# Optimization experiments

Hardware: AMD Instinct MI355X
Metric: run time of the kernel (lower is better)

The kernel has to match this reference:

```python
import jax, jax.numpy as jnp
import numpy as np

N_NODES = 50000
N_EDGES = 1000000
N_GRAPHS = 256
ORIG = 92
ATOM = 64
NBR = 41
EPS = 1e-5


def _bn_train(h, gamma, beta):
    # BatchNorm1d in training mode: batch stats, biased variance
    mu = h.mean(axis=0)
    var = jnp.var(h, axis=0)
    return (h - mu) * jax.lax.rsqrt(var + EPS) * gamma + beta


def setup_inputs() -> dict:
    key = jax.random.key(0)
    ks = jax.random.split(key, 16)
    inp = {
        "x": jax.random.normal(ks[0], (N_NODES, ORIG), dtype=jnp.float32),
        "edge_attr": jax.random.normal(ks[1], (N_EDGES, NBR), dtype=jnp.float32),
        "lower_f": jax.random.normal(ks[2], (N_NODES, ATOM), dtype=jnp.float32),
        "edge_index": jax.random.randint(ks[3], (2, N_EDGES), 0, N_NODES, dtype=jnp.int32),
        "batch": jnp.sort(jax.random.randint(ks[4], (N_NODES,), 0, N_GRAPHS, dtype=jnp.int32)),
        # params
        "emb_W": jax.random.normal(ks[5], (ORIG, ATOM), dtype=jnp.float32) / np.sqrt(ORIG),
        "emb_b": jnp.zeros((ATOM,), dtype=jnp.float32),
        "fc_W": jax.random.normal(ks[6], (2 * ATOM + NBR, 2 * ATOM), dtype=jnp.float32) / np.sqrt(2 * ATOM + NBR),
        "fc_b": jnp.zeros((2 * ATOM,), dtype=jnp.float32),
        "bn1_g": jnp.ones((2 * ATOM,), dtype=jnp.float32),
        "bn1_b": jnp.zeros((2 * ATOM,), dtype=jnp.float32),
        "bn2_g": jnp.ones((ATOM,), dtype=jnp.float32),
        "bn2_b": jnp.zeros((ATOM,), dtype=jnp.float32),
        "att_W": jax.random.normal(ks[7], (ATOM, 1), dtype=jnp.float32) / np.sqrt(ATOM),
        "att_b": jnp.zeros((1,), dtype=jnp.float32),
        "out_W": jax.random.normal(ks[8], (ATOM, 1), dtype=jnp.float32) / np.sqrt(ATOM),
        "out_b": jnp.zeros((1,), dtype=jnp.float32),
    }
    return inp


def reference(x, edge_attr, lower_f, emb_W, emb_b, fc_W, fc_b, bn1_g, bn1_b,
              bn2_g, bn2_b, att_W, att_b, out_W, out_b, edge_index, batch):
    # embedding + lower-level features
    atom_fea = x @ emb_W + emb_b + lower_f  # [N, ATOM]

    # CGConv: gather endpoints, concat with edge features
    src, dst = edge_index[0], edge_index[1]
    total = jnp.concatenate([atom_fea[src], atom_fea[dst], edge_attr], axis=-1)  # [E, 2A+NBR]
    gated = _bn_train(total @ fc_W + fc_b, bn1_g, bn1_b)  # [E, 2A]
    nbr_filter, nbr_core = gated[:, :ATOM], gated[:, ATOM:]
    msg = jax.nn.sigmoid(nbr_filter) * jax.nn.softplus(nbr_core)  # [E, A]
    summed = jax.ops.segment_sum(msg, src, num_segments=N_NODES)  # [N, A]
    atom_out = _bn_train(summed, bn2_g, bn2_b)

    # SiLU + attentional aggregation per graph
    h = jax.nn.silu(atom_out)  # [N, A]
    logits = (h @ att_W + att_b)[:, 0]  # [N]
    seg_max = jax.ops.segment_max(logits, batch, num_segments=N_GRAPHS)
    e = jnp.exp(logits - seg_max[batch])
    denom = jax.ops.segment_sum(e, batch, num_segments=N_GRAPHS)
    alpha = e / denom[batch]  # [N]
    crys = jax.ops.segment_sum(alpha[:, None] * h, batch, num_segments=N_GRAPHS)  # [G, A]
    crys_fea = crys @ out_W + out_b  # [G, 1]
    return atom_out, crys_fea
```

## Files before the change

### kernel.cpp

```cpp
#include <hip/hip_runtime.h>
#include <math.h>

#define NN 50000
#define NE 1000000
#define NG 256
#define ORIGD 92
#define NBRD 41
#define NSPREAD 32
#define SCAN_B 256

typedef unsigned short u16;
typedef __attribute__((ext_vector_type(8))) short short8;
typedef __attribute__((ext_vector_type(4))) float f32x4;

#define OFF_AFB     0
#define OFF_SUMMED  1600000
#define OFF_WT      4800000
#define OFF_BN1SPR  4812288
#define OFF_BN1SC   4820480
#define OFF_BN2ACC  4820736
#define OFF_BN2SC   4820864
#define OFF_ELOG    4820992
#define OFF_SEGMAX  4870992
#define OFF_DENOM   4871248
#define OFF_CNT     4871504
#define OFF_PTR     4921504
#define OFF_HEAD    4971504
#define OFF_BSUM    5021504
#define OFF_BOFS    5021760
#define OFF_EIDX    5022016
#define OFF_H       6022016
#define OFF_T2_END  70022016
#define OFF_P       70022016
#define OFF_T3_END  82822016

__device__ __forceinline__ u16 f2b(float f) {
    unsigned u = __float_as_uint(f);
    return (u16)((u + 0x7FFFu + ((u >> 16) & 1u)) >> 16);
}
__device__ __forceinline__ float b2f(u16 u) {
    return __uint_as_float(((unsigned)u) << 16);
}
__device__ __forceinline__ float gate(float f, float cc) {
    float sig = __builtin_amdgcn_rcpf(1.f + __expf(-f));
    float sp  = fmaxf(cc, 0.f) + __logf(1.f + __expf(-fabsf(cc)));
    return sig * sp;
}
__device__ __forceinline__ float fsilu(float x) {
    return x * __builtin_amdgcn_rcpf(1.f + __expf(-x));
}

__global__ __launch_bounds__(256) void k_embed(
    const float* __restrict__ x, const float* __restrict__ lf,
    const float* __restrict__ W, const float* __restrict__ b,
    u16* __restrict__ afb)
{
    int gid = blockIdx.x * 256 + threadIdx.x;
    int n = gid >> 6, c = gid & 63;
    const float* xr = x + (long)n * ORIGD;
    float acc = b[c] + lf[gid];
#pragma unroll 4
    for (int k = 0; k < ORIGD; k++)
        acc = fmaf(xr[k], W[k * 64 + c], acc);
    afb[gid] = f2b(acc);
}

__global__ void k_prepw(const float* __restrict__ fcW, u16* __restrict__ wT)
{
    int i = blockIdx.x * 256 + threadIdx.x;
    int j = i / 192, k = i - j * 192;
    wT[i] = (k < 169) ? f2b(fcW[k * 128 + j]) : (u16)0;
}

__global__ void k_prepw2(const float* __restrict__ fcW, u16* __restrict__ wT3,
                         u16* __restrict__ wP)
{
    int i = blockIdx.x * 256 + threadIdx.x;
    if (i < 8192) {
        int j = i >> 6, k = i & 63;
        wT3[i] = (k < NBRD) ? f2b(fcW[(128 + k) * 128 + j]) : (u16)0;
    } else {
        int i2 = i - 8192;
        int j = i2 >> 6, k = i2 & 63;
        int row = (j < 128) ? k : (64 + k);
        wP[i2] = f2b(fcW[row * 128 + (j & 127)]);
    }
}

__global__ __launch_bounds__(256) void k_pnode(
    const u16* __restrict__ afb, const u16* __restrict__ wP, float* __restrict__ P)
{
    __shared__ __align__(16) u16 sB[64 * 72];
    const int tid = threadIdx.x;
    const int n0 = blockIdx.x * 64;

    for (int i = tid; i < 512; i += 256) {
        int r = i >> 3, c = i & 7;
        int n = n0 + r;
        short8 v = {0,0,0,0,0,0,0,0};
        if (n < NN) v = *(const short8*)(afb + (long)n * 64 + c * 8);
        *(short8*)(sB + r * 72 + c * 8) = v;
    }
    __syncthreads();

    const int lane = tid & 63, w = tid >> 6;
    const int n16 = lane & 15, quad = lane >> 4;
    short8 A[4][2];
#pragma unroll
    for (int m = 0; m < 4; m++) {
        const u16* base = wP + (16 * (w + 4 * m) + n16) * 64 + quad * 8;
        A[m][0] = *(const short8*)(base);
        A[m][1] = *(const short8*)(base + 32);
    }
    for (int t = 0; t < 4; t++) {
        const u16* row = sB + (16 * t + n16) * 72 + quad * 8;
        short8 b0 = *(const short8*)(row);
        short8 b1 = *(const short8*)(row + 32);
        int n = n0 + 16 * t + n16;
#pragma unroll
        for (int m = 0; m < 4; m++) {
            f32x4 acc = {0.f, 0.f, 0.f, 0.f};
            acc = __builtin_amdgcn_mfma_f32_16x16x32_bf16(A[m][0], b0, acc, 0, 0, 0);
            acc = __builtin_amdgcn_mfma_f32_16x16x32_bf16(A[m][1], b1, acc, 0, 0, 0);
            if (n < NN) {
                int j = 16 * (w + 4 * m) + 4 * quad;
                *(f32x4*)(P + (long)n * 256 + j) = acc;
            }
        }
    }
}

__global__ void k_hist(const int* __restrict__ ei, int* __restrict__ cnt)
{
    int e = blockIdx.x * 256 + threadIdx.x;
    if (e < NE) atomicAdd(&cnt[ei[e]], 1);
}

__global__ void k_partial(const int* __restrict__ cnt, int* __restrict__ lofs,
                          int* __restrict__ bsum)
{
    __shared__ int sd[SCAN_B];
    int t = threadIdx.x, b = blockIdx.x, n = b * SCAN_B + t;
    int v = (n < NN) ? cnt[n] : 0;
    sd[t] = v; __syncthreads();
    for (int o = 1; o < SCAN_B; o <<= 1) {
        int x = (t >= o) ? sd[t - o] : 0;
        __syncthreads();
        sd[t] += x;
        __syncthreads();
    }
    if (n < NN) lofs[n] = sd[t] - v;
    if (t == SCAN_B - 1) bsum[b] = sd[t];
}

__global__ void k_scanb(const int* __restrict__ bsum, int* __restrict__ bofs, int nb)
{
    __shared__ int sd[256];
    int t = threadIdx.x;
    int v = (t < nb) ? bsum[t] : 0;
    sd[t] = v; __syncthreads();
    for (int o = 1; o < 256; o <<= 1) {
        int x = (t >= o) ? sd[t - o] : 0;
        __syncthreads();
        sd[t] += x;
        __syncthreads();
    }
    bofs[t] = sd[t] - v;
}

__global__ void k_addofs(int* __restrict__ ptr, const int* __restrict__ bofs,
                         int* __restrict__ head)
{
    int n = blockIdx.x * 256 + threadIdx.x;
    if (n < NN) {
        int p = ptr[n] + bofs[n >> 8];
        ptr[n] = p; head[n] = p;
    }
}

__global__ void k_fill(const int* __restrict__ ei, int* __restrict__ head,
                       int* __restrict__ eidx)
{
    int e = blockIdx.x * 256 + threadIdx.x;
    if (e < NE) {
        int pos = atomicAdd(&head[ei[e]], 1);
        eidx[pos] = e;
    }
}

__global__ __launch_bounds__(256) void k_gemm_h2(
    const float* __restrict__ ea, const int* __restrict__ ei,
    const u16* __restrict__ wT3, const float* __restrict__ P,
    u16* __restrict__ h, float* __restrict__ spread)
{
    __shared__ __align__(16) u16 sTl[64 * 72];
    __shared__ int sSrc[64], sDst[64];
    const int tid = threadIdx.x;
    const int e0 = blockIdx.x * 64;

    if (tid < 64) sSrc[tid] = ei[e0 + tid];
    else if (tid < 128) sDst[tid - 64] = ei[NE + e0 + tid - 64];

    for (int i = tid; i < 64 * 64; i += 256) {
        int e = i >> 6, c = i & 63;
        float v = (c < NBRD) ? ea[(long)(e0 + e) * NBRD + c] : 0.f;
        sTl[e * 72 + c] = f2b(v);
    }
    __syncthreads();

    const int lane = tid & 63, w = tid >> 6;
    const int n16 = lane & 15, quad = lane >> 4;

    short8 A0[2], A1[2];
    {
        const u16* b0 = wT3 + (16 * w + n16) * 64 + quad * 8;
        const u16* b1 = wT3 + (16 * (w + 4) + n16) * 64 + quad * 8;
        A0[0] = *(const short8*)(b0);  A0[1] = *(const short8*)(b0 + 32);
        A1[0] = *(const short8*)(b1);  A1[1] = *(const short8*)(b1 + 32);
    }

    const int j0 = 16 * w + 4 * quad;
    float s0[4] = {0,0,0,0}, q0[4] = {0,0,0,0}, s1[4] = {0,0,0,0}, q1[4] = {0,0,0,0};

    for (int t = 0; t < 4; t++) {
        const int ge16 = 16 * t + n16;
        const int src = sSrc[ge16], dst = sDst[ge16];
        const float* pS = P + (long)src * 256;
        const float* pD = P + (long)dst * 256 + 128;
        f32x4 g0 = *(const f32x4*)(pS + j0);
        f32x4 g1 = *(const f32x4*)(pS + 64 + j0);
        f32x4 g2 = *(const f32x4*)(pD + j0);
        f32x4 g3 = *(const f32x4*)(pD + 64 + j0);

        const u16* row = sTl + ge16 * 72 + quad * 8;
        short8 b0 = *(const short8*)(row);
        short8 b1 = *(const short8*)(row + 32);
        f32x4 acc0 = {0.f, 0.f, 0.f, 0.f}, acc1 = {0.f, 0.f, 0.f, 0.f};
        acc0 = __builtin_amdgcn_mfma_f32_16x16x32_bf16(A0[0], b0, acc0, 0, 0, 0);
        acc0 = __builtin_amdgcn_mfma_f32_16x16x32_bf16(A0[1], b1, acc0, 0, 0, 0);
        acc1 = __builtin_amdgcn_mfma_f32_16x16x32_bf16(A1[0], b0, acc1, 0, 0, 0);
        acc1 = __builtin_amdgcn_mfma_f32_16x16x32_bf16(A1[1], b1, acc1, 0, 0, 0);

        u16 hv0[4], hv1[4];
#pragma unroll
        for (int r = 0; r < 4; r++) {
            float u0 = acc0[r] + g0[r] + g2[r];
            float u1 = acc1[r] + g1[r] + g3[r];
            s0[r] += u0; q0[r] = fmaf(u0, u0, q0[r]);
            s1[r] += u1; q1[r] = fmaf(u1, u1, q1[r]);
            hv0[r] = f2b(u0); hv1[r] = f2b(u1);
        }
        int ge = e0 + ge16;
        u16* hp = h + (long)ge * 128 + j0;
        ushort4 v0 = make_ushort4(hv0[0], hv0[1], hv0[2], hv0[3]);
        ushort4 v1 = make_ushort4(hv1[0], hv1[1], hv1[2], hv1[3]);
        *(ushort4*)hp = v0;
        *(ushort4*)(hp + 64) = v1;
    }

#pragma unroll
    for (int m = 1; m < 16; m <<= 1) {
#pragma unroll
        for (int r = 0; r < 4; r++) {
            s0[r] += __shfl_xor(s0[r], m); q0[r] += __shfl_xor(q0[r], m);
            s1[r] += __shfl_xor(s1[r], m); q1[r] += __shfl_xor(q1[r], m);
        }
    }
    if (n16 == 0) {
        float* sp = spread + (blockIdx.x & (NSPREAD - 1)) * 256;
#pragma unroll
        for (int r = 0; r < 4; r++) {
            atomicAdd(sp + j0 + r,       s0[r]);
            atomicAdd(sp + 128 + j0 + r, q0[r]);
            atomicAdd(sp + 64 + j0 + r,  s1[r]);
            atomicAdd(sp + 192 + j0 + r, q1[r]);
        }
    }
}

__global__ __launch_bounds__(256) void k_gemm_h(
    const u16* __restrict__ afb, const float* __restrict__ ea,
    const int* __restrict__ ei, const u16* __restrict__ wT,
    u16* __restrict__ h, float* __restrict__ spread)
{
    __shared__ __align__(16) u16 sTl[64 * 200];
    __shared__ int sSrc[64], sDst[64];
    const int tid = threadIdx.x;
    const int e0 = blockIdx.x * 64;

    if (tid < 64) sSrc[tid] = ei[e0 + tid];
    else if (tid < 128) sDst[tid - 64] = ei[NE + e0 + tid - 64];
    __syncthreads();

    for (int i = tid; i < 1024; i += 256) {
        int e = i >> 4, q = i & 15;
        const u16* g = (q < 8) ? (afb + (long)sSrc[e] * 64 + q * 8)
                               : (afb + (long)sDst[e] * 64 + (q - 8) * 8);
        *(short8*)(sTl + e * 200 + q * 8) = *(const short8*)g;
    }
    for (int i = tid; i < 64 * 64; i += 256) {
        int e = i >> 6, c = i & 63;
        float v = (c < NBRD) ? ea[(long)(e0 + e) * NBRD + c] : 0.f;
        sTl[e * 200 + 128 + c] = f2b(v);
    }
    __syncthreads();

    const int lane = tid & 63, w = tid >> 6;
    const int n16 = lane & 15, quad = lane >> 4;

    short8 A0[6], A1[6];
    {
        const u16* b0 = wT + (16 * w + n16) * 192 + quad * 8;
        const u16* b1 = wT + (16 * (w + 4) + n16) * 192 + quad * 8;
#pragma unroll
        for (int ks = 0; ks < 6; ks++) {
            A0[ks] = *(const short8*)(b0 + ks * 32);
            A1[ks] = *(const short8*)(b1 + ks * 32);
        }
    }

    const int j0 = 16 * w + 4 * quad;
    float s0[4] = {0,0,0,0}, q0[4] = {0,0,0,0}, s1[4] = {0,0,0,0}, q1[4] = {0,0,0,0};

    for (int t = 0; t < 4; t++) {
        const u16* row = sTl + (16 * t + n16) * 200 + quad * 8;
        f32x4 acc0 = {0.f, 0.f, 0.f, 0.f}, acc1 = {0.f, 0.f, 0.f, 0.f};
#pragma unroll
        for (int ks = 0; ks < 6; ks++) {
            short8 b = *(const short8*)(row + ks * 32);
            acc0 = __builtin_amdgcn_mfma_f32_16x16x32_bf16(A0[ks], b, acc0, 0, 0, 0);
            acc1 = __builtin_amdgcn_mfma_f32_16x16x32_bf16(A1[ks], b, acc1, 0, 0, 0);
        }
#pragma unroll
        for (int r = 0; r < 4; r++) {
            s0[r] += acc0[r]; q0[r] = fmaf(acc0[r], acc0[r], q0[r]);
            s1[r] += acc1[r]; q1[r] = fmaf(acc1[r], acc1[r], q1[r]);
        }
        int ge = e0 + 16 * t + n16;
        u16* hp = h + (long)ge * 128 + j0;
        ushort4 v0 = make_ushort4(f2b(acc0[0]), f2b(acc0[1]), f2b(acc0[2]), f2b(acc0[3]));
        ushort4 v1 = make_ushort4(f2b(acc1[0]), f2b(acc1[1]), f2b(acc1[2]), f2b(acc1[3]));
        *(ushort4*)hp = v0;
        *(ushort4*)(hp + 64) = v1;
    }

#pragma unroll
    for (int m = 1; m < 16; m <<= 1) {
#pragma unroll
        for (int r = 0; r < 4; r++) {
            s0[r] += __shfl_xor(s0[r], m); q0[r] += __shfl_xor(q0[r], m);
            s1[r] += __shfl_xor(s1[r], m); q1[r] += __shfl_xor(q1[r], m);
        }
    }
    if (n16 == 0) {
        float* sp = spread + (blockIdx.x & (NSPREAD - 1)) * 256;
#pragma unroll
        for (int r = 0; r < 4; r++) {
            atomicAdd(sp + j0 + r,       s0[r]);
            atomicAdd(sp + 128 + j0 + r, q0[r]);
            atomicAdd(sp + 64 + j0 + r,  s1[r]);
            atomicAdd(sp + 192 + j0 + r, q1[r]);
        }
    }
}

template <int MODE>
__global__ __launch_bounds__(256) void k_gemm(
    const u16* __restrict__ afb, const float* __restrict__ ea,
    const int* __restrict__ ei, const u16* __restrict__ wT,
    const float* __restrict__ sc, float* __restrict__ outbuf)
{
    __shared__ __align__(16) u16 sTl[64 * 200];
    __shared__ int sSrc[64], sDst[64];
    const int tid = threadIdx.x;
    const int e0 = blockIdx.x * 64;

    if (tid < 64) sSrc[tid] = ei[e0 + tid];
    else if (tid < 128) sDst[tid - 64] = ei[NE + e0 + tid - 64];
    __syncthreads();
    for (int i = tid; i < 1024; i += 256) {
        int e = i >> 4, q = i & 15;
        const u16* g = (q < 8) ? (afb + (long)sSrc[e] * 64 + q * 8)
                               : (afb + (long)sDst[e] * 64 + (q - 8) * 8);
        *(short8*)(sTl + e * 200 + q * 8) = *(const short8*)g;
    }
    for (int i = tid; i < 64 * 64; i += 256) {
        int e = i >> 6, c = i & 63;
        float v = (c < NBRD) ? ea[(long)(e0 + e) * NBRD + c] : 0.f;
        sTl[e * 200 + 128 + c] = f2b(v);
    }
    __syncthreads();

    const int lane = tid & 63, w = tid >> 6;
    const int n16 = lane & 15, quad = lane >> 4;
    short8 A0[6], A1[6];
    {
        const u16* b0 = wT + (16 * w + n16) * 192 + quad * 8;
        const u16* b1 = wT + (16 * (w + 4) + n16) * 192 + quad * 8;
#pragma unroll
        for (int ks = 0; ks < 6; ks++) {
            A0[ks] = *(const short8*)(b0 + ks * 32);
            A1[ks] = *(const short8*)(b1 + ks * 32);
        }
    }
    const int j0 = 16 * w + 4 * quad;
    float s0[4] = {0,0,0,0}, q0[4] = {0,0,0,0}, s1[4] = {0,0,0,0}, q1[4] = {0,0,0,0};
    float scf[4], shf[4], scc[4], shc[4];
    if (MODE == 1) {
#pragma unroll
        for (int r = 0; r < 4; r++) {
            scf[r] = sc[j0 + r];        shf[r] = sc[128 + j0 + r];
            scc[r] = sc[64 + j0 + r];   shc[r] = sc[192 + j0 + r];
        }
    }
    for (int t = 0; t < 4; t++) {
        const u16* row = sTl + (16 * t + n16) * 200 + quad * 8;
        f32x4 acc0 = {0.f, 0.f, 0.f, 0.f}, acc1 = {0.f, 0.f, 0.f, 0.f};
#pragma unroll
        for (int ks = 0; ks < 6; ks++) {
            short8 b = *(const short8*)(row + ks * 32);
            acc0 = __builtin_amdgcn_mfma_f32_16x16x32_bf16(A0[ks], b, acc0, 0, 0, 0);
            acc1 = __builtin_amdgcn_mfma_f32_16x16x32_bf16(A1[ks], b, acc1, 0, 0, 0);
        }
        if (MODE == 0) {
#pragma unroll
            for (int r = 0; r < 4; r++) {
                s0[r] += acc0[r]; q0[r] = fmaf(acc0[r], acc0[r], q0[r]);
                s1[r] += acc1[r]; q1[r] = fmaf(acc1[r], acc1[r], q1[r]);
            }
        } else {
            int src = sSrc[16 * t + n16];
            float* dst = outbuf + (long)src * 64 + j0;
#pragma unroll
            for (int r = 0; r < 4; r++) {
                float f  = fmaf(acc0[r], scf[r], shf[r]);
                float cc = fmaf(acc1[r], scc[r], shc[r]);
                atomicAdd(dst + r, gate(f, cc));
            }
        }
    }
    if (MODE == 0) {
#pragma unroll
        for (int m = 1; m < 16; m <<= 1) {
#pragma unroll
            for (int r = 0; r < 4; r++) {
                s0[r] += __shfl_xor(s0[r], m); q0[r] += __shfl_xor(q0[r], m);
                s1[r] += __shfl_xor(s1[r], m); q1[r] += __shfl_xor(q1[r], m);
            }
        }
        if (n16 == 0) {
            float* sp = outbuf + (blockIdx.x & (NSPREAD - 1)) * 256;
#pragma unroll
            for (int r = 0; r < 4; r++) {
                atomicAdd(sp + j0 + r,       s0[r]);
                atomicAdd(sp + 128 + j0 + r, q0[r]);
                atomicAdd(sp + 64 + j0 + r,  s1[r]);
                atomicAdd(sp + 192 + j0 + r, q1[r]);
            }
        }
    }
}

__global__ void k_bn1fin(const float* __restrict__ spread,
                         const float* __restrict__ g, const float* __restrict__ b,
                         float* __restrict__ sc)
{
    int c = threadIdx.x;
    float s = 0.f, q = 0.f;
    for (int k = 0; k < NSPREAD; k++) { s += spread[k * 256 + c]; q += spread[k * 256 + 128 + c]; }
    float mean_acc = s / (float)NE;
    float var = q / (float)NE - mean_acc * mean_acc;
    float scale = g[c] * rsqrtf(var + 1e-5f);
    sc[c] = scale;
    sc[128 + c] = b[c] - mean_acc * scale;
}

__global__ __launch_bounds__(256) void k_scatter(
    const u16* __restrict__ h, const int* __restrict__ ptr,
    const int* __restrict__ cnt, const int* __restrict__ eidx,
    const float* __restrict__ sc, float* __restrict__ summed)
{
    int tid = threadIdx.x;
    int n = blockIdx.x * 4 + (tid >> 6);
    int l = tid & 63;
    int es = l & 7, cg = l >> 3;

    float4 a0 = *(const float4*)(sc + cg * 8);
    float4 a1 = *(const float4*)(sc + cg * 8 + 4);
    float4 b0 = *(const float4*)(sc + 128 + cg * 8);
    float4 b1 = *(const float4*)(sc + 128 + cg * 8 + 4);
    float4 c0 = *(const float4*)(sc + 64 + cg * 8);
    float4 c1 = *(const float4*)(sc + 64 + cg * 8 + 4);
    float4 d0 = *(const float4*)(sc + 192 + cg * 8);
    float4 d1 = *(const float4*)(sc + 192 + cg * 8 + 4);
    float scf[8] = {a0.x,a0.y,a0.z,a0.w,a1.x,a1.y,a1.z,a1.w};
    float shf[8] = {b0.x,b0.y,b0.z,b0.w,b1.x,b1.y,b1.z,b1.w};
    float scc[8] = {c0.x,c0.y,c0.z,c0.w,c1.x,c1.y,c1.z,c1.w};
    float shc[8] = {d0.x,d0.y,d0.z,d0.w,d1.x,d1.y,d1.z,d1.w};

    int p0 = ptr[n], deg = cnt[n];
    float acc[8] = {0,0,0,0,0,0,0,0};
    for (int i = 0; i < deg; i += 8) {
        int idx = i + es;
        bool valid = idx < deg;
        int e = eidx[p0 + (valid ? idx : 0)];
        const u16* hr = h + (long)e * 128;
        short8 f8 = *(const short8*)(hr + cg * 8);
        short8 c8 = *(const short8*)(hr + 64 + cg * 8);
#pragma unroll
        for (int j = 0; j < 8; j++) {
            float f  = fmaf(b2f((u16)f8[j]), scf[j], shf[j]);
            float cc = fmaf(b2f((u16)c8[j]), scc[j], shc[j]);
            float g  = gate(f, cc);
            acc[j] += valid ? g : 0.f;
        }
    }
#pragma unroll
    for (int m = 1; m < 8; m <<= 1)
#pragma unroll
        for (int j = 0; j < 8; j++) acc[j] += __shfl_xor(acc[j], m);
    if (es == 0) {
        float* sp = summed + (long)n * 64 + cg * 8;
        float4 v0 = {acc[0], acc[1], acc[2], acc[3]};
        float4 v1 = {acc[4], acc[5], acc[6], acc[7]};
        *(float4*)sp = v0;
        *(float4*)(sp + 4) = v1;
    }
}

__global__ __launch_bounds__(256) void k_bn2stats(const float* __restrict__ summed,
                                                  float* __restrict__ acc2)
{
    int tid = threadIdx.x; int c = tid & 63; int sub = tid >> 6;
    float s = 0.f, q = 0.f;
    for (int r = blockIdx.x * 4 + sub; r < NN; r += 4 * 128) {
        float v = summed[(long)r * 64 + c]; s += v; q = fmaf(v, v, q);
    }
    __shared__ float rs[256], rq[256];
    rs[tid] = s; rq[tid] = q; __syncthreads();
    if (tid < 64) {
        s = rs[tid] + rs[tid + 64] + rs[tid + 128] + rs[tid + 192];
        q = rq[tid] + rq[tid + 64] + rq[tid + 128] + rq[tid + 192];
        atomicAdd(&acc2[tid], s);
        atomicAdd(&acc2[64 + tid], q);
    }
}

__global__ void k_bn2fin(const float* __restrict__ acc2,
                         const float* __restrict__ g, const float* __restrict__ b,
                         float* __restrict__ sc2, const float* __restrict__ outb,
                         float* __restrict__ out)
{
    int c = threadIdx.x;
    if (c < 64) {
        float mean = acc2[c] / (float)NN;
        float var = acc2[64 + c] / (float)NN - mean * mean;
        float scale = g[c] * rsqrtf(var + 1e-5f);
        sc2[c] = scale;
        sc2[64 + c] = b[c] - mean * scale;
    }
    out[(long)NN * 64 + c] = outb[0];
}

__global__ __launch_bounds__(256) void k_nodepost(
    const float* __restrict__ summed, const float* __restrict__ sc2,
    const float* __restrict__ attW, const float* __restrict__ attb,
    const int* __restrict__ batch, float* __restrict__ out,
    float* __restrict__ elog, unsigned* __restrict__ segmax)
{
    int tid = threadIdx.x; int n = blockIdx.x * 4 + (tid >> 6); int c = tid & 63;
    float v = summed[(long)n * 64 + c];
    float ao = fmaf(v, sc2[c], sc2[64 + c]);
    out[(long)n * 64 + c] = ao;
    float h = fsilu(ao);
    float p = h * attW[c];
#pragma unroll
    for (int off = 32; off; off >>= 1) p += __shfl_down(p, off, 64);
    if (c == 0) {
        float logit = p + attb[0];
        elog[n] = logit;
        unsigned u = __float_as_uint(logit);
        u = (u & 0x80000000u) ? ~u : (u | 0x80000000u);
        atomicMax(&segmax[batch[n]], u);
    }
}

__global__ void k_denom(const int* __restrict__ batch,
                        const unsigned* __restrict__ segmax,
                        float* __restrict__ elog, float* __restrict__ denom)
{
    int n = blockIdx.x * 256 + threadIdx.x;
    if (n >= NN) return;
    int b = batch[n];
    unsigned u = segmax[b];
    u = (u & 0x80000000u) ? (u & 0x7FFFFFFFu) : ~u;
    float e = __expf(elog[n] - __uint_as_float(u));
    elog[n] = e;
    atomicAdd(&denom[b], e);
}

__global__ __launch_bounds__(256) void k_crys(
    const float* __restrict__ atom_out, const float* __restrict__ elog,
    const float* __restrict__ denom, const int* __restrict__ batch,
    const float* __restrict__ outW, float* __restrict__ out)
{
    int tid = threadIdx.x; int n = blockIdx.x * 4 + (tid >> 6); int l = tid & 63;
    int b = batch[n];
    float alpha = elog[n] / denom[b];
    float ao = atom_out[(long)n * 64 + l];
    float p = fsilu(ao) * outW[l];
#pragma unroll
    for (int off = 32; off; off >>= 1) p += __shfl_down(p, off, 64);
    if (l == 0) atomicAdd(&out[(long)NN * 64 + b], alpha * p);
}

extern "C" void kernel_launch(void* const* d_in, const int* in_sizes, int n_in,
                              void* d_out, int out_size, void* d_ws, size_t ws_size,
                              hipStream_t stream)
{
    const float* x    = (const float*)d_in[0];
    const float* eatt = (const float*)d_in[1];
    const float* lf   = (const float*)d_in[2];
    const int*   ei   = (const int*)d_in[3];
    const int*   batch= (const int*)d_in[4];
    const float* embW = (const float*)d_in[5];
    const float* embB = (const float*)d_in[6];
    const float* fcW  = (const float*)d_in[7];
    const float* bn1g = (const float*)d_in[9];
    const float* bn1b = (const float*)d_in[10];
    const float* bn2g = (const float*)d_in[11];
    const float* bn2b = (const float*)d_in[12];
    const float* attW = (const float*)d_in[13];
    const float* attB = (const float*)d_in[14];
    const float* outW = (const float*)d_in[15];
    const float* outB = (const float*)d_in[16];
    float* out = (float*)d_out;
    float* ws  = (float*)d_ws;

    u16* afb  = (u16*)(ws + OFF_AFB);
    u16* wT   = (u16*)(ws + OFF_WT);
    int* cnt  = (int*)(ws + OFF_CNT);
    int* ptr  = (int*)(ws + OFF_PTR);
    int* head = (int*)(ws + OFF_HEAD);
    int* bsum = (int*)(ws + OFF_BSUM);
    int* bofs = (int*)(ws + OFF_BOFS);
    int* eidx = (int*)(ws + OFF_EIDX);
    u16* h    = (u16*)(ws + OFF_H);

    const bool t3 = ws_size >= (size_t)OFF_T3_END * sizeof(float);
    const bool t2 = ws_size >= (size_t)OFF_T2_END * sizeof(float);

    k_embed<<<12500, 256, 0, stream>>>(x, lf, embW, embB, afb);

    if (t3) {
        u16* wT3 = wT;
        u16* wP  = wT + 8192;
        float* P = ws + OFF_P;
        k_prepw2<<<96, 256, 0, stream>>>(fcW, wT3, wP);
        hipMemsetAsync(ws + OFF_BN1SPR, 0,
                       (size_t)(OFF_PTR - OFF_BN1SPR) * sizeof(float), stream);
        k_hist<<<(NE + 255) / 256, 256, 0, stream>>>(ei, cnt);
        k_partial<<<(NN + SCAN_B - 1) / SCAN_B, SCAN_B, 0, stream>>>(cnt, ptr, bsum);
        k_scanb<<<1, 256, 0, stream>>>(bsum, bofs, (NN + SCAN_B - 1) / SCAN_B);
        k_addofs<<<(NN + 255) / 256, 256, 0, stream>>>(ptr, bofs, head);
        k_fill<<<(NE + 255) / 256, 256, 0, stream>>>(ei, head, eidx);
        k_pnode<<<(NN + 63) / 64, 256, 0, stream>>>(afb, wP, P);
        k_gemm_h2<<<NE / 64, 256, 0, stream>>>(eatt, ei, wT3, P, h, ws + OFF_BN1SPR);
        k_bn1fin<<<1, 128, 0, stream>>>(ws + OFF_BN1SPR, bn1g, bn1b, ws + OFF_BN1SC);
        k_scatter<<<NN / 4, 256, 0, stream>>>(h, ptr, cnt, eidx, ws + OFF_BN1SC,
                                              ws + OFF_SUMMED);
    } else if (t2) {
        k_prepw<<<96, 256, 0, stream>>>(fcW, wT);
        hipMemsetAsync(ws + OFF_BN1SPR, 0,
                       (size_t)(OFF_PTR - OFF_BN1SPR) * sizeof(float), stream);
        k_hist<<<(NE + 255) / 256, 256, 0, stream>>>(ei, cnt);
        k_partial<<<(NN + SCAN_B - 1) / SCAN_B, SCAN_B, 0, stream>>>(cnt, ptr, bsum);
        k_scanb<<<1, 256, 0, stream>>>(bsum, bofs, (NN + SCAN_B - 1) / SCAN_B);
        k_addofs<<<(NN + 255) / 256, 256, 0, stream>>>(ptr, bofs, head);
        k_fill<<<(NE + 255) / 256, 256, 0, stream>>>(ei, head, eidx);
        k_gemm_h<<<NE / 64, 256, 0, stream>>>(afb, eatt, ei, wT, h, ws + OFF_BN1SPR);
        k_bn1fin<<<1, 128, 0, stream>>>(ws + OFF_BN1SPR, bn1g, bn1b, ws + OFF_BN1SC);
        k_scatter<<<NN / 4, 256, 0, stream>>>(h, ptr, cnt, eidx, ws + OFF_BN1SC,
                                              ws + OFF_SUMMED);
    } else {
        k_prepw<<<96, 256, 0, stream>>>(fcW, wT);
        hipMemsetAsync(ws + OFF_SUMMED, 0,
                       (size_t)(OFF_PTR - OFF_SUMMED) * sizeof(float), stream);
        k_gemm<0><<<NE / 64, 256, 0, stream>>>(afb, eatt, ei, wT, ws + OFF_BN1SC,
                                               ws + OFF_BN1SPR);
        k_bn1fin<<<1, 128, 0, stream>>>(ws + OFF_BN1SPR, bn1g, bn1b, ws + OFF_BN1SC);
        k_gemm<1><<<NE / 64, 256, 0, stream>>>(afb, eatt, ei, wT, ws + OFF_BN1SC,
                                               ws + OFF_SUMMED);
    }

    k_bn2stats<<<128, 256, 0, stream>>>(ws + OFF_SUMMED, ws + OFF_BN2ACC);
    k_bn2fin<<<1, 256, 0, stream>>>(ws + OFF_BN2ACC, bn2g, bn2b, ws + OFF_BN2SC,
                                    outB, out);
    k_nodepost<<<12500, 256, 0, stream>>>(ws + OFF_SUMMED, ws + OFF_BN2SC, attW, attB,
                                          batch, out, ws + OFF_ELOG,
                                          (unsigned*)(ws + OFF_SEGMAX));
    k_denom<<<196, 256, 0, stream>>>(batch, (const unsigned*)(ws + OFF_SEGMAX),
                                     ws + OFF_ELOG, ws + OFF_DENOM);
    k_crys<<<12500, 256, 0, stream>>>(out, ws + OFF_ELOG, ws + OFF_DENOM, batch,
                                      outW, out);
}
```

Baseline: 1.241 ms.

## Compute edge GEMM in src-sorted order and pre-convert edge_attr to bf16

Adds a new path that writes h in CSR (src-sorted) order, so the scatter reads contiguous rows directly instead of indirecting through eidx. Edge attributes are first converted to a padded 48-wide bf16 buffer, so the GEMM loads aligned short8 vectors per edge. The fill kernel now also records src and dst per sorted position. The gathers in the GEMM become irregular over eaB and the dst rows of P, and the path needs roughly 100 MB more workspace; if that workspace is not available, the old path runs.

```diff
diff --git a/kernel.cpp b/kernel.cpp
--- a/kernel.cpp
+++ b/kernel.cpp
@@ -33,6 +33,10 @@
 #define OFF_T2_END  70022016
 #define OFF_P       70022016
 #define OFF_T3_END  82822016
+#define OFF_SRCC    82822016
+#define OFF_DSTC    83822016
+#define OFF_EAB     84822016
+#define OFF_T4_END  108822016
 
 __device__ __forceinline__ u16 f2b(float f) {
     unsigned u = __float_as_uint(f);
@@ -87,6 +91,23 @@
     }
 }
 
+__global__ __launch_bounds__(256) void k_prepea(const float* __restrict__ ea,
+                                                u16* __restrict__ eaB)
+{
+    int gid = blockIdx.x * 256 + threadIdx.x;
+    if (gid >= NE * 6) return;
+    int e = gid / 6, q = gid - e * 6;
+    const float* row = ea + (long)e * NBRD;
+    int c0 = q * 8;
+    short8 v;
+#pragma unroll
+    for (int j = 0; j < 8; j++) {
+        int c = c0 + j;
+        v[j] = (c < NBRD) ? (short)f2b(row[c]) : (short)0;
+    }
+    *(short8*)(eaB + (long)e * 48 + c0) = v;
+}
+
 __global__ __launch_bounds__(256) void k_pnode(
     const u16* __restrict__ afb, const u16* __restrict__ wP, float* __restrict__ P)
 {
@@ -188,6 +209,103 @@
     }
 }
 
+__global__ void k_fill2(const int* __restrict__ ei, int* __restrict__ head,
+                        int* __restrict__ eidx, int* __restrict__ srcC,
+                        int* __restrict__ dstC)
+{
+    int e = blockIdx.x * 256 + threadIdx.x;
+    if (e < NE) {
+        int s = ei[e];
+        int pos = atomicAdd(&head[s], 1);
+        eidx[pos] = e;
+        srcC[pos] = s;
+        dstC[pos] = ei[NE + e];
+    }
+}
+
+__global__ __launch_bounds__(256) void k_gemm_h3(
+    const u16* __restrict__ eaB, const int* __restrict__ eidx,
+    const int* __restrict__ srcC, const int* __restrict__ dstC,
+    const u16* __restrict__ wT3, const float* __restrict__ P,
+    u16* __restrict__ h, float* __restrict__ spread)
+{
+    const int tid = threadIdx.x;
+    const int e0 = blockIdx.x * 64;
+    const int lane = tid & 63, w = tid >> 6;
+    const int n16 = lane & 15, quad = lane >> 4;
+
+    short8 A0[2], A1[2];
+    {
+        const u16* a0 = wT3 + (16 * w + n16) * 64 + quad * 8;
+        const u16* a1 = wT3 + (16 * (w + 4) + n16) * 64 + quad * 8;
+        A0[0] = *(const short8*)(a0);  A0[1] = *(const short8*)(a0 + 32);
+        A1[0] = *(const short8*)(a1);  A1[1] = *(const short8*)(a1 + 32);
+    }
+
+    const int j0 = 16 * w + 4 * quad;
+    const short8 bz = {0,0,0,0,0,0,0,0};
+    float s0[4] = {0,0,0,0}, q0[4] = {0,0,0,0}, s1[4] = {0,0,0,0}, q1[4] = {0,0,0,0};
+
+    for (int t = 0; t < 4; t++) {
+        const int pos = e0 + 16 * t + n16;
+        const int e   = eidx[pos];
+        const int src = srcC[pos];
+        const int dst = dstC[pos];
+
+        const u16* er = eaB + (long)e * 48;
+        short8 b0 = *(const short8*)(er + quad * 8);
+        short8 b1 = bz;
+        if (quad < 2) b1 = *(const short8*)(er + 32 + quad * 8);
+
+        const float* pS = P + (long)src * 256;
+        const float* pD = P + (long)dst * 256 + 128;
+        f32x4 g0 = *(const f32x4*)(pS + j0);
+        f32x4 g1 = *(const f32x4*)(pS + 64 + j0);
+        f32x4 g2 = *(const f32x4*)(pD + j0);
+        f32x4 g3 = *(const f32x4*)(pD + 64 + j0);
+
+        f32x4 acc0 = {0.f, 0.f, 0.f, 0.f}, acc1 = {0.f, 0.f, 0.f, 0.f};
+        acc0 = __builtin_amdgcn_mfma_f32_16x16x32_bf16(A0[0], b0, acc0, 0, 0, 0);
+        acc0 = __builtin_amdgcn_mfma_f32_16x16x32_bf16(A0[1], b1, acc0, 0, 0, 0);
+        acc1 = __builtin_amdgcn_mfma_f32_16x16x32_bf16(A1[0], b0, acc1, 0, 0, 0);
+        acc1 = __builtin_amdgcn_mfma_f32_16x16x32_bf16(A1[1], b1, acc1, 0, 0, 0);
+
+        u16 hv0[4], hv1[4];
+#pragma unroll
+        for (int r = 0; r < 4; r++) {
+            float u0 = acc0[r] + g0[r] + g2[r];
+            float u1 = acc1[r] + g1[r] + g3[r];
+            s0[r] += u0; q0[r] = fmaf(u0, u0, q0[r]);
+            s1[r] += u1; q1[r] = fmaf(u1, u1, q1[r]);
+            hv0[r] = f2b(u0); hv1[r] = f2b(u1);
+        }
+        u16* hp = h + (long)pos * 128 + j0;
+        ushort4 v0 = make_ushort4(hv0[0], hv0[1], hv0[2], hv0[3]);
+        ushort4 v1 = make_ushort4(hv1[0], hv1[1], hv1[2], hv1[3]);
+        *(ushort4*)hp = v0;
+        *(ushort4*)(hp + 64) = v1;
+    }
+
+#pragma unroll
+    for (int m = 1; m < 16; m <<= 1) {
+#pragma unroll
+        for (int r = 0; r < 4; r++) {
+            s0[r] += __shfl_xor(s0[r], m); q0[r] += __shfl_xor(q0[r], m);
+            s1[r] += __shfl_xor(s1[r], m); q1[r] += __shfl_xor(q1[r], m);
+        }
+    }
+    if (n16 == 0) {
+        float* sp = spread + (blockIdx.x & (NSPREAD - 1)) * 256;
+#pragma unroll
+        for (int r = 0; r < 4; r++) {
+            atomicAdd(sp + j0 + r,       s0[r]);
+            atomicAdd(sp + 128 + j0 + r, q0[r]);
+            atomicAdd(sp + 64 + j0 + r,  s1[r]);
+            atomicAdd(sp + 192 + j0 + r, q1[r]);
+        }
+    }
+}
+
 __global__ __launch_bounds__(256) void k_gemm_h2(
     const float* __restrict__ ea, const int* __restrict__ ei,
     const u16* __restrict__ wT3, const float* __restrict__ P,
@@ -473,6 +591,59 @@
     float scale = g[c] * rsqrtf(var + 1e-5f);
     sc[c] = scale;
     sc[128 + c] = b[c] - mean_acc * scale;
+}
+
+__global__ __launch_bounds__(256) void k_scatter2(
+    const u16* __restrict__ h, const int* __restrict__ ptr,
+    const int* __restrict__ cnt, const float* __restrict__ sc,
+    float* __restrict__ summed)
+{
+    int tid = threadIdx.x;
+    int n = blockIdx.x * 4 + (tid >> 6);
+    int l = tid & 63;
+    int es = l & 7, cg = l >> 3;
+
+    float4 a0 = *(const float4*)(sc + cg * 8);
+    float4 a1 = *(const float4*)(sc + cg * 8 + 4);
+    float4 b0 = *(const float4*)(sc + 128 + cg * 8);
+    float4 b1 = *(const float4*)(sc + 128 + cg * 8 + 4);
+    float4 c0 = *(const float4*)(sc + 64 + cg * 8);
+    float4 c1 = *(const float4*)(sc + 64 + cg * 8 + 4);
+    float4 d0 = *(const float4*)(sc + 192 + cg * 8);
+    float4 d1 = *(const float4*)(sc + 192 + cg * 8 + 4);
+    float scf[8] = {a0.x,a0.y,a0.z,a0.w,a1.x,a1.y,a1.z,a1.w};
+    float shf[8] = {b0.x,b0.y,b0.z,b0.w,b1.x,b1.y,b1.z,b1.w};
+    float scc[8] = {c0.x,c0.y,c0.z,c0.w,c1.x,c1.y,c1.z,c1.w};
+    float shc[8] = {d0.x,d0.y,d0.z,d0.w,d1.x,d1.y,d1.z,d1.w};
+
+    int p0 = ptr[n], deg = cnt[n];
+    float acc[8] = {0,0,0,0,0,0,0,0};
+    for (int i = 0; i < deg; i += 8) {
+        int idx = i + es;
+        bool valid = idx < deg;
+        int row = p0 + (valid ? idx : 0);
+        const u16* hr = h + (long)row * 128;
+        short8 f8 = *(const short8*)(hr + cg * 8);
+        short8 c8 = *(const short8*)(hr + 64 + cg * 8);
+#pragma unroll
+        for (int j = 0; j < 8; j++) {
+            float f  = fmaf(b2f((u16)f8[j]), scf[j], shf[j]);
+            float cc = fmaf(b2f((u16)c8[j]), scc[j], shc[j]);
+            float g  = gate(f, cc);
+            acc[j] += valid ? g : 0.f;
+        }
+    }
+#pragma unroll
+    for (int m = 1; m < 8; m <<= 1)
+#pragma unroll
+        for (int j = 0; j < 8; j++) acc[j] += __shfl_xor(acc[j], m);
+    if (es == 0) {
+        float* sp = summed + (long)n * 64 + cg * 8;
+        float4 v0 = {acc[0], acc[1], acc[2], acc[3]};
+        float4 v1 = {acc[4], acc[5], acc[6], acc[7]};
+        *(float4*)sp = v0;
+        *(float4*)(sp + 4) = v1;
+    }
 }
 
 __global__ __launch_bounds__(256) void k_scatter(
@@ -647,12 +818,35 @@
     int* eidx = (int*)(ws + OFF_EIDX);
     u16* h    = (u16*)(ws + OFF_H);
 
+    const bool t4 = ws_size >= (size_t)OFF_T4_END * sizeof(float);
     const bool t3 = ws_size >= (size_t)OFF_T3_END * sizeof(float);
     const bool t2 = ws_size >= (size_t)OFF_T2_END * sizeof(float);
 
     k_embed<<<12500, 256, 0, stream>>>(x, lf, embW, embB, afb);
 
-    if (t3) {
+    if (t4) {
+        u16* wT3  = wT;
+        u16* wP   = wT + 8192;
+        float* P  = ws + OFF_P;
+        int* srcC = (int*)(ws + OFF_SRCC);
+        int* dstC = (int*)(ws + OFF_DSTC);
+        u16* eaB  = (u16*)(ws + OFF_EAB);
+        k_prepw2<<<96, 256, 0, stream>>>(fcW, wT3, wP);
+        hipMemsetAsync(ws + OFF_BN1SPR, 0,
+                       (size_t)(OFF_PTR - OFF_BN1SPR) * sizeof(float), stream);
+        k_prepea<<<(NE * 6 + 255) / 256, 256, 0, stream>>>(eatt, eaB);
+        k_hist<<<(NE + 255) / 256, 256, 0, stream>>>(ei, cnt);
+        k_partial<<<(NN + SCAN_B - 1) / SCAN_B, SCAN_B, 0, stream>>>(cnt, ptr, bsum);
+        k_scanb<<<1, 256, 0, stream>>>(bsum, bofs, (NN + SCAN_B - 1) / SCAN_B);
+        k_addofs<<<(NN + 255) / 256, 256, 0, stream>>>(ptr, bofs, head);
+        k_fill2<<<(NE + 255) / 256, 256, 0, stream>>>(ei, head, eidx, srcC, dstC);
+        k_pnode<<<(NN + 63) / 64, 256, 0, stream>>>(afb, wP, P);
+        k_gemm_h3<<<NE / 64, 256, 0, stream>>>(eaB, eidx, srcC, dstC, wT3, P, h,
+                                               ws + OFF_BN1SPR);
+        k_bn1fin<<<1, 128, 0, stream>>>(ws + OFF_BN1SPR, bn1g, bn1b, ws + OFF_BN1SC);
+        k_scatter2<<<NN / 4, 256, 0, stream>>>(h, ptr, cnt, ws + OFF_BN1SC,
+                                               ws + OFF_SUMMED);
+    } else if (t3) {
         u16* wT3 = wT;
         u16* wP  = wT + 8192;
         float* P = ws + OFF_P;
```

New measurement: 1.212 ms. 2.3% less time.
